# Kernel tuning notes

Hardware: AMD Instinct MI355X
Metric: run time of the kernel (lower is better)

## Reference

```python
import jax, jax.numpy as jnp
import numpy as np

C_M, C_Z, C = 256, 128, 32
N_SEQ, N_RES = 128, 256


def setup_inputs() -> dict:
    key = jax.random.key(0)
    ks = jax.random.split(key, 9)
    s = 0.02
    return {
        "m": jax.random.normal(ks[0], (N_SEQ, N_RES, C_M), dtype=jnp.float32),
        "ln_w": jnp.ones((C_M,), dtype=jnp.float32),
        "ln_b": jnp.zeros((C_M,), dtype=jnp.float32),
        "w1": jax.random.normal(ks[1], (C, C_M), dtype=jnp.float32) * s,
        "b1": jnp.zeros((C,), dtype=jnp.float32),
        "w2": jax.random.normal(ks[2], (C, C_M), dtype=jnp.float32) * s,
        "b2": jnp.zeros((C,), dtype=jnp.float32),
        "wo": jax.random.normal(ks[3], (C_Z, C * C), dtype=jnp.float32) * s,
        "bo": jnp.zeros((C_Z,), dtype=jnp.float32),
    }


def reference(m, ln_w, ln_b, w1, b1, w2, b2, wo, bo):
    n_seq = m.shape[-3]
    # LayerNorm over c_m
    mu = jnp.mean(m, axis=-1, keepdims=True)
    var = jnp.mean(jnp.square(m - mu), axis=-1, keepdims=True)
    mn = (m - mu) * jax.lax.rsqrt(var + 1e-5) * ln_w + ln_b
    # dual projections to c channels: [s, i, c]
    a = jnp.einsum('sim,cm->sic', mn, w1) + b1
    b = jnp.einsum('sjm,dm->sjd', mn, w2) + b2
    # outer product mean contracted over sequence axis: [i, j, c, d]
    o = jnp.einsum('sic,sjd->ijcd', a, b)
    o = o.reshape(o.shape[0], o.shape[1], C * C)
    # output projection and mean over sequences
    z = (jnp.einsum('ijk,zk->ijz', o, wo) + bo) / n_seq
    return z
```

## Files before the change

### kernel.cpp

```cpp
#include <hip/hip_runtime.h>
#include <hip/hip_bf16.h>
#include <stdint.h>

#define N_RES 256
#define CMDIM 256

typedef __attribute__((ext_vector_type(8))) short bf16x8;
typedef __attribute__((ext_vector_type(4))) float f32x4;
typedef __attribute__((ext_vector_type(2))) unsigned int u32x2;

__device__ __forceinline__ unsigned short f32_to_bf16(float f) {
    union { float f; unsigned int u; } v; v.f = f;
    unsigned int u = v.u;
    return (unsigned short)((u + 0x7FFFu + ((u >> 16) & 1u)) >> 16);
}

__device__ __forceinline__ int swz5(int x) {
    return ((x >> 2) & 7) | (((x >> 5) & 1) << 3) | ((x & 1) << 4);
}


__global__ __launch_bounds__(256) void k_ln_proj(
    const float* __restrict__ m, const float* __restrict__ lnw, const float* __restrict__ lnb,
    const float* __restrict__ w1, const float* __restrict__ b1,
    const float* __restrict__ w2, const float* __restrict__ b2,
    const float* __restrict__ wo,
    unsigned short* __restrict__ A2f, unsigned short* __restrict__ B2f,
    unsigned short* __restrict__ wof)
{
    __shared__ unsigned short mn[32 * 256];
    __shared__ unsigned short stg[2048];
    int b = blockIdx.x;
    int i = b >> 2, sblk = b & 3;
    int tid = threadIdx.x;
    int wv = tid >> 6, lane = tid & 63;
    int quad = lane >> 4, l15 = lane & 15;

    if (tid < 128) {
        int t = b * 128 + tid;
        int zo = t >> 10, k = t & 1023;
        int addr = ((zo >> 4) * 32 + (k >> 5)) * 512 + ((k >> 3) & 3) * 128 + (zo & 15) * 8 + (k & 7);
        wof[addr] = f32_to_bf16(wo[t]);
    }

    f32x4 lw = *(const f32x4*)(lnw + lane * 4);
    f32x4 lb = *(const f32x4*)(lnb + lane * 4);

    #pragma unroll
    for (int r = 0; r < 8; ++r) {
        int sl = wv * 8 + r;
        int s = sblk * 32 + sl;
        const float* row = m + ((size_t)s * N_RES + i) * CMDIM;
        f32x4 x = *(const f32x4*)(row + lane * 4);
        float s1 = x[0] + x[1] + x[2] + x[3];
        float s2 = x[0]*x[0] + x[1]*x[1] + x[2]*x[2] + x[3]*x[3];
        #pragma unroll
        for (int off = 32; off; off >>= 1) {
            s1 += __shfl_xor(s1, off);
            s2 += __shfl_xor(s2, off);
        }
        float mu = s1 * (1.0f / 256.0f);
        float var = s2 * (1.0f / 256.0f) - mu * mu;
        float rstd = rsqrtf(var + 1e-5f);
        float n0 = (x[0] - mu) * rstd * lw[0] + lb[0];
        float n1 = (x[1] - mu) * rstd * lw[1] + lb[1];
        float n2 = (x[2] - mu) * rstd * lw[2] + lb[2];
        float n3 = (x[3] - mu) * rstd * lw[3] + lb[3];
        unsigned int p0 = (unsigned)f32_to_bf16(n0) | ((unsigned)f32_to_bf16(n1) << 16);
        unsigned int p1 = (unsigned)f32_to_bf16(n2) | ((unsigned)f32_to_bf16(n3) << 16);
        int chunk = lane >> 1;
        int pos = (chunk & 16) | ((chunk ^ sl) & 15);
        unsigned int* dst = (unsigned int*)((char*)mn + sl * 512 + pos * 16 + (lane & 1) * 8);
        dst[0] = p0; dst[1] = p1;
    }

    const float* wrow = (wv < 2) ? (w1 + (size_t)(wv * 16 + l15) * 256)
                                 : (w2 + (size_t)((wv - 2) * 16 + l15) * 256);
    bf16x8 af[8];
    #pragma unroll
    for (int ks = 0; ks < 8; ++ks) {
        f32x4 lo = *(const f32x4*)(wrow + ks * 32 + quad * 8);
        f32x4 hi = *(const f32x4*)(wrow + ks * 32 + quad * 8 + 4);
        bf16x8 f;
        f[0] = (short)f32_to_bf16(lo[0]);
        f[1] = (short)f32_to_bf16(lo[1]);
        f[2] = (short)f32_to_bf16(lo[2]);
        f[3] = (short)f32_to_bf16(lo[3]);
        f[4] = (short)f32_to_bf16(hi[0]);
        f[5] = (short)f32_to_bf16(hi[1]);
        f[6] = (short)f32_to_bf16(hi[2]);
        f[7] = (short)f32_to_bf16(hi[3]);
        af[ks] = f;
    }

    __syncthreads();

    f32x4 acc[2];
    acc[0] = (f32x4){0.f, 0.f, 0.f, 0.f};
    acc[1] = (f32x4){0.f, 0.f, 0.f, 0.f};
    #pragma unroll
    for (int ks = 0; ks < 8; ++ks) {
        #pragma unroll
        for (int nb = 0; nb < 2; ++nb) {
            int sl = nb * 16 + l15;
            int chunk = ks * 4 + quad;
            int pos = (chunk & 16) | ((chunk ^ sl) & 15);
            bf16x8 bf = *(const bf16x8*)((char*)mn + sl * 512 + pos * 16);
            acc[nb] = __builtin_amdgcn_mfma_f32_16x16x32_bf16(af[ks], bf, acc[nb], 0, 0, 0);
        }
    }

    const float* bsrc = (wv < 2) ? b1 : b2;
    f32x4 bias = *(const f32x4*)(bsrc + (wv & 1) * 16 + quad * 4);
    unsigned short* sbase = stg + (wv >> 1) * 1024 + (wv & 1) * 512 + quad * 32;
    #pragma unroll
    for (int nb = 0; nb < 2; ++nb) {
        int sl = nb * 16 + l15;
        int soff = ((sl >> 3) & 3) * 128 + (sl & 7);
        #pragma unroll
        for (int reg = 0; reg < 4; ++reg)
            sbase[soff + reg * 8] = f32_to_bf16(acc[nb][reg] + bias[reg]);
    }
    __syncthreads();

    int part = tid >> 7, blk = (tid >> 6) & 1, l = tid & 63;
    unsigned short* gdst = (part ? B2f : A2f) + ((i * 2 + blk) * 4 + sblk) * 512 + l * 8;
    *(bf16x8*)gdst = *(const bf16x8*)(stg + tid * 8);
}

__global__ __launch_bounds__(256, 2) void k_fused(
    const unsigned short* __restrict__ A2f, const unsigned short* __restrict__ B2f,
    const unsigned short* __restrict__ wof, const float* __restrict__ bo,
    float* __restrict__ out)
{
    __shared__ char olds[65536];
    int bid = blockIdx.x;
    int sb = (bid & 7) * 256 + (bid >> 3);
    int bx = sb & 63, by = sb >> 6;
    int tid = threadIdx.x, wv = tid >> 6, lane = tid & 63;
    int quad = lane >> 4, l15 = lane & 15;
    int wm = wv & 1, wn = wv >> 1;

    const unsigned short* Abase = A2f + (size_t)((bx * 8 + wn * 4) * 4) * 512 + lane * 8;

    bf16x8 bn[4][4];
    #pragma unroll
    for (int nb = 0; nb < 4; ++nb)
        #pragma unroll
        for (int ks = 0; ks < 4; ++ks)
            bn[ks][nb] = *(const bf16x8*)(Abase + (size_t)(nb * 4 + ks) * 512);

    #pragma unroll
    for (int pass = 0; pass < 2; ++pass) {
        const unsigned short* Bbase = B2f + (size_t)((by * 16 + pass * 8 + wm * 4) * 4) * 512 + lane * 8;
        f32x4 acc[4][4];
        #pragma unroll
        for (int a = 0; a < 4; ++a)
            #pragma unroll
            for (int b = 0; b < 4; ++b) acc[a][b] = (f32x4){0.f, 0.f, 0.f, 0.f};

        bf16x8 am[4][4];
        #pragma unroll
        for (int mb = 0; mb < 4; ++mb)
            #pragma unroll
            for (int ks = 0; ks < 4; ++ks)
                am[ks][mb] = *(const bf16x8*)(Bbase + (size_t)(mb * 4 + ks) * 512);

        __builtin_amdgcn_s_setprio(1);
        #pragma unroll
        for (int ks = 0; ks < 4; ++ks)
            #pragma unroll
            for (int mb = 0; mb < 4; ++mb)
                #pragma unroll
                for (int nb = 0; nb < 4; ++nb)
                    acc[mb][nb] = __builtin_amdgcn_mfma_f32_16x16x32_bf16(am[ks][mb], bn[ks][nb], acc[mb][nb], 0, 0, 0);
        __builtin_amdgcn_s_setprio(0);

        #pragma unroll
        for (int mb = 0; mb < 4; ++mb) {
            int m_ = wm * 64 + mb * 16 + quad * 4;
            int d0 = m_ & 31;
            int jl = pass * 4 + (m_ >> 5);
            #pragma unroll
            for (int nb = 0; nb < 4; ++nb) {
                int n_ = wn * 64 + nb * 16 + l15;
                int c = n_ & 31, il = n_ >> 5;
                int pair = il * 8 + jl;
                int e0 = c * 32 + d0;
                int chunk = e0 >> 3;
                int phys = pair ^ swz5(chunk);
                f32x4 a4 = acc[mb][nb];
                unsigned int p0 = (unsigned)f32_to_bf16(a4[0]) | ((unsigned)f32_to_bf16(a4[1]) << 16);
                unsigned int p1 = (unsigned)f32_to_bf16(a4[2]) | ((unsigned)f32_to_bf16(a4[3]) << 16);
                u32x2 pv = {p0, p1};
                *(u32x2*)(olds + chunk * 512 + phys * 16 + (e0 & 7) * 2) = pv;
            }
        }
    }

    int zg = wv;
    const unsigned short* wbase = wof + (size_t)(zg * 64) * 512 + lane * 8;

    bf16x8 af2[6][4], bfr2[6][4];
    #pragma unroll
    for (int p = 0; p < 5; ++p)
        #pragma unroll
        for (int zb = 0; zb < 2; ++zb)
            #pragma unroll
            for (int h = 0; h < 2; ++h)
                af2[p][zb * 2 + h] = *(const bf16x8*)(wbase + (size_t)(zb * 32 + 2 * p + h) * 512);
    __builtin_amdgcn_sched_barrier(0);

    __syncthreads();

    #pragma unroll
    for (int p = 0; p < 5; ++p)
        #pragma unroll
        for (int pb = 0; pb < 2; ++pb)
            #pragma unroll
            for (int h = 0; h < 2; ++h) {
                int kt = 2 * p + h;
                int pair = pb * 16 + l15;
                int chunk = kt * 4 + quad;
                int phys = pair ^ swz5(chunk);
                bfr2[p][pb * 2 + h] = *(const bf16x8*)(olds + chunk * 512 + phys * 16);
            }
    __builtin_amdgcn_sched_barrier(0);

    f32x4 acc2[2][2];
    #pragma unroll
    for (int a = 0; a < 2; ++a)
        #pragma unroll
        for (int b = 0; b < 2; ++b) acc2[a][b] = (f32x4){0.f, 0.f, 0.f, 0.f};

    #pragma unroll
    for (int s = 0; s < 16; ++s) {
        int slot = s % 6;
        if (s < 11) {
            int t = s + 5, ps = t % 6;
            #pragma unroll
            for (int zb = 0; zb < 2; ++zb)
                #pragma unroll
                for (int h = 0; h < 2; ++h)
                    af2[ps][zb * 2 + h] = *(const bf16x8*)(wbase + (size_t)(zb * 32 + 2 * t + h) * 512);
            #pragma unroll
            for (int pb = 0; pb < 2; ++pb)
                #pragma unroll
                for (int h = 0; h < 2; ++h) {
                    int kt = 2 * t + h;
                    int pair = pb * 16 + l15;
                    int chunk = kt * 4 + quad;
                    int phys = pair ^ swz5(chunk);
                    bfr2[ps][pb * 2 + h] = *(const bf16x8*)(olds + chunk * 512 + phys * 16);
                }
            __builtin_amdgcn_sched_barrier(0);
        }
        __builtin_amdgcn_s_setprio(1);
        #pragma unroll
        for (int h = 0; h < 2; ++h)
            #pragma unroll
            for (int zb = 0; zb < 2; ++zb)
                #pragma unroll
                for (int pb = 0; pb < 2; ++pb)
                    acc2[zb][pb] = __builtin_amdgcn_mfma_f32_16x16x32_bf16(
                        af2[slot][zb * 2 + h], bfr2[slot][pb * 2 + h], acc2[zb][pb], 0, 0, 0);
        __builtin_amdgcn_s_setprio(0);
    }

    #pragma unroll
    for (int zb = 0; zb < 2; ++zb) {
        int zo = zg * 32 + zb * 16 + quad * 4;
        f32x4 b4 = *(const f32x4*)(bo + zo);
        #pragma unroll
        for (int pb = 0; pb < 2; ++pb) {
            int pair = pb * 16 + l15;
            int i = bx * 4 + (pair >> 3);
            int j = by * 8 + (pair & 7);
            f32x4 v;
            #pragma unroll
            for (int reg = 0; reg < 4; ++reg)
                v[reg] = (acc2[zb][pb][reg] + b4[reg]) * (1.0f / 128.0f);
            *(f32x4*)(out + ((size_t)(i * 256 + j)) * 128 + zo) = v;
        }
    }
}

extern "C" void kernel_launch(void* const* d_in, const int* in_sizes, int n_in,
                              void* d_out, int out_size, void* d_ws, size_t ws_size,
                              hipStream_t stream) {
    const float* m   = (const float*)d_in[0];
    const float* lnw = (const float*)d_in[1];
    const float* lnb = (const float*)d_in[2];
    const float* w1  = (const float*)d_in[3];
    const float* b1  = (const float*)d_in[4];
    const float* w2  = (const float*)d_in[5];
    const float* b2  = (const float*)d_in[6];
    const float* wo  = (const float*)d_in[7];
    const float* bo  = (const float*)d_in[8];
    float* out = (float*)d_out;
    char* ws = (char*)d_ws;

    unsigned short* wof = (unsigned short*)(ws + 32768);
    unsigned short* A2f = (unsigned short*)(ws + 32768 + 262144);
    unsigned short* B2f = (unsigned short*)(ws + 32768 + 262144 + 2097152);

    hipLaunchKernelGGL(k_ln_proj, dim3(1024), dim3(256), 0, stream,
                       m, lnw, lnb, w1, b1, w2, b2, wo, A2f, B2f, wof);
    hipLaunchKernelGGL(k_fused, dim3(2048), dim3(256), 0, stream,
                       A2f, B2f, wof, bo, out);
}
```

Before: 143.4 us.

## Double workgroup to 512 threads, split outer-product passes and K across waves

The fused kernel now uses 8 waves instead of 4. Each wave handles one of the two outer-product passes at once rather than looping over them. The output projection is split along K between wave pairs, and the partial sums are reduced through shared memory. The old software-pipelined, register-rotated weight prefetch is replaced by loading all 16 weight fragments into registers up front. This aims for more parallelism per block, at the cost of extra syncs, a shared-memory reduction, higher register pressure at launch_bounds(512,2), and less latency hiding.

```diff
diff --git a/kernel.cpp b/kernel.cpp
--- a/kernel.cpp
+++ b/kernel.cpp
@@ -128,7 +128,7 @@
     *(bf16x8*)gdst = *(const bf16x8*)(stg + tid * 8);
 }
 
-__global__ __launch_bounds__(256, 2) void k_fused(
+__global__ __launch_bounds__(512, 2) void k_fused(
     const unsigned short* __restrict__ A2f, const unsigned short* __restrict__ B2f,
     const unsigned short* __restrict__ wof, const float* __restrict__ bo,
     float* __restrict__ out)
@@ -139,93 +139,70 @@
     int bx = sb & 63, by = sb >> 6;
     int tid = threadIdx.x, wv = tid >> 6, lane = tid & 63;
     int quad = lane >> 4, l15 = lane & 15;
-    int wm = wv & 1, wn = wv >> 1;
+    int pass = wv >> 2, wm = (wv >> 1) & 1, wn = wv & 1;
 
     const unsigned short* Abase = A2f + (size_t)((bx * 8 + wn * 4) * 4) * 512 + lane * 8;
-
-    bf16x8 bn[4][4];
+    const unsigned short* Bbase = B2f + (size_t)((by * 16 + pass * 8 + wm * 4) * 4) * 512 + lane * 8;
+
+    bf16x8 bn[4][4], am[4][4];
     #pragma unroll
     for (int nb = 0; nb < 4; ++nb)
         #pragma unroll
         for (int ks = 0; ks < 4; ++ks)
             bn[ks][nb] = *(const bf16x8*)(Abase + (size_t)(nb * 4 + ks) * 512);
-
-    #pragma unroll
-    for (int pass = 0; pass < 2; ++pass) {
-        const unsigned short* Bbase = B2f + (size_t)((by * 16 + pass * 8 + wm * 4) * 4) * 512 + lane * 8;
-        f32x4 acc[4][4];
-        #pragma unroll
-        for (int a = 0; a < 4; ++a)
-            #pragma unroll
-            for (int b = 0; b < 4; ++b) acc[a][b] = (f32x4){0.f, 0.f, 0.f, 0.f};
-
-        bf16x8 am[4][4];
+    #pragma unroll
+    for (int mb = 0; mb < 4; ++mb)
+        #pragma unroll
+        for (int ks = 0; ks < 4; ++ks)
+            am[ks][mb] = *(const bf16x8*)(Bbase + (size_t)(mb * 4 + ks) * 512);
+
+    f32x4 acc[4][4];
+    #pragma unroll
+    for (int a = 0; a < 4; ++a)
+        #pragma unroll
+        for (int b = 0; b < 4; ++b) acc[a][b] = (f32x4){0.f, 0.f, 0.f, 0.f};
+
+    __builtin_amdgcn_s_setprio(1);
+    #pragma unroll
+    for (int ks = 0; ks < 4; ++ks)
         #pragma unroll
         for (int mb = 0; mb < 4; ++mb)
             #pragma unroll
-            for (int ks = 0; ks < 4; ++ks)
-                am[ks][mb] = *(const bf16x8*)(Bbase + (size_t)(mb * 4 + ks) * 512);
-
-        __builtin_amdgcn_s_setprio(1);
-        #pragma unroll
-        for (int ks = 0; ks < 4; ++ks)
-            #pragma unroll
-            for (int mb = 0; mb < 4; ++mb)
-                #pragma unroll
-                for (int nb = 0; nb < 4; ++nb)
-                    acc[mb][nb] = __builtin_amdgcn_mfma_f32_16x16x32_bf16(am[ks][mb], bn[ks][nb], acc[mb][nb], 0, 0, 0);
-        __builtin_amdgcn_s_setprio(0);
-
-        #pragma unroll
-        for (int mb = 0; mb < 4; ++mb) {
-            int m_ = wm * 64 + mb * 16 + quad * 4;
-            int d0 = m_ & 31;
-            int jl = pass * 4 + (m_ >> 5);
-            #pragma unroll
-            for (int nb = 0; nb < 4; ++nb) {
-                int n_ = wn * 64 + nb * 16 + l15;
-                int c = n_ & 31, il = n_ >> 5;
-                int pair = il * 8 + jl;
-                int e0 = c * 32 + d0;
-                int chunk = e0 >> 3;
-                int phys = pair ^ swz5(chunk);
-                f32x4 a4 = acc[mb][nb];
-                unsigned int p0 = (unsigned)f32_to_bf16(a4[0]) | ((unsigned)f32_to_bf16(a4[1]) << 16);
-                unsigned int p1 = (unsigned)f32_to_bf16(a4[2]) | ((unsigned)f32_to_bf16(a4[3]) << 16);
-                u32x2 pv = {p0, p1};
-                *(u32x2*)(olds + chunk * 512 + phys * 16 + (e0 & 7) * 2) = pv;
-            }
-        }
-    }
-
-    int zg = wv;
-    const unsigned short* wbase = wof + (size_t)(zg * 64) * 512 + lane * 8;
-
-    bf16x8 af2[6][4], bfr2[6][4];
-    #pragma unroll
-    for (int p = 0; p < 5; ++p)
-        #pragma unroll
-        for (int zb = 0; zb < 2; ++zb)
-            #pragma unroll
-            for (int h = 0; h < 2; ++h)
-                af2[p][zb * 2 + h] = *(const bf16x8*)(wbase + (size_t)(zb * 32 + 2 * p + h) * 512);
-    __builtin_amdgcn_sched_barrier(0);
-
-    __syncthreads();
-
-    #pragma unroll
-    for (int p = 0; p < 5; ++p)
-        #pragma unroll
-        for (int pb = 0; pb < 2; ++pb)
-            #pragma unroll
-            for (int h = 0; h < 2; ++h) {
-                int kt = 2 * p + h;
-                int pair = pb * 16 + l15;
-                int chunk = kt * 4 + quad;
-                int phys = pair ^ swz5(chunk);
-                bfr2[p][pb * 2 + h] = *(const bf16x8*)(olds + chunk * 512 + phys * 16);
-            }
-    __builtin_amdgcn_sched_barrier(0);
+            for (int nb = 0; nb < 4; ++nb)
+                acc[mb][nb] = __builtin_amdgcn_mfma_f32_16x16x32_bf16(am[ks][mb], bn[ks][nb], acc[mb][nb], 0, 0, 0);
+    __builtin_amdgcn_s_setprio(0);
+
+    #pragma unroll
+    for (int mb = 0; mb < 4; ++mb) {
+        int m_ = wm * 64 + mb * 16 + quad * 4;
+        int d0 = m_ & 31;
+        int jl = pass * 4 + (m_ >> 5);
+        #pragma unroll
+        for (int nb = 0; nb < 4; ++nb) {
+            int n_ = wn * 64 + nb * 16 + l15;
+            int c = n_ & 31, il = n_ >> 5;
+            int pair = il * 8 + jl;
+            int e0 = c * 32 + d0;
+            int chunk = e0 >> 3;
+            int phys = pair ^ swz5(chunk);
+            f32x4 a4 = acc[mb][nb];
+            unsigned int p0 = (unsigned)f32_to_bf16(a4[0]) | ((unsigned)f32_to_bf16(a4[1]) << 16);
+            unsigned int p1 = (unsigned)f32_to_bf16(a4[2]) | ((unsigned)f32_to_bf16(a4[3]) << 16);
+            u32x2 pv = {p0, p1};
+            *(u32x2*)(olds + chunk * 512 + phys * 16 + (e0 & 7) * 2) = pv;
+        }
+    }
+
+    int zg = wv >> 1, kh = wv & 1, kt0 = kh * 16;
+    const unsigned short* wbase = wof + lane * 8;
+    bf16x8 wreg[2][16];
+    #pragma unroll
+    for (int zb = 0; zb < 2; ++zb)
+        #pragma unroll
+        for (int kt = 0; kt < 16; ++kt)
+            wreg[zb][kt] = *(const bf16x8*)(wbase + (size_t)(((2 * zg + zb) * 32) + kt0 + kt) * 512);
+
+    __syncthreads();
 
     f32x4 acc2[2][2];
     #pragma unroll
@@ -234,53 +211,50 @@
         for (int b = 0; b < 2; ++b) acc2[a][b] = (f32x4){0.f, 0.f, 0.f, 0.f};
 
     #pragma unroll
-    for (int s = 0; s < 16; ++s) {
-        int slot = s % 6;
-        if (s < 11) {
-            int t = s + 5, ps = t % 6;
-            #pragma unroll
-            for (int zb = 0; zb < 2; ++zb)
-                #pragma unroll
-                for (int h = 0; h < 2; ++h)
-                    af2[ps][zb * 2 + h] = *(const bf16x8*)(wbase + (size_t)(zb * 32 + 2 * t + h) * 512);
-            #pragma unroll
-            for (int pb = 0; pb < 2; ++pb)
-                #pragma unroll
-                for (int h = 0; h < 2; ++h) {
-                    int kt = 2 * t + h;
-                    int pair = pb * 16 + l15;
-                    int chunk = kt * 4 + quad;
-                    int phys = pair ^ swz5(chunk);
-                    bfr2[ps][pb * 2 + h] = *(const bf16x8*)(olds + chunk * 512 + phys * 16);
-                }
-            __builtin_amdgcn_sched_barrier(0);
-        }
-        __builtin_amdgcn_s_setprio(1);
-        #pragma unroll
-        for (int h = 0; h < 2; ++h)
-            #pragma unroll
-            for (int zb = 0; zb < 2; ++zb)
-                #pragma unroll
-                for (int pb = 0; pb < 2; ++pb)
-                    acc2[zb][pb] = __builtin_amdgcn_mfma_f32_16x16x32_bf16(
-                        af2[slot][zb * 2 + h], bfr2[slot][pb * 2 + h], acc2[zb][pb], 0, 0, 0);
-        __builtin_amdgcn_s_setprio(0);
-    }
-
-    #pragma unroll
-    for (int zb = 0; zb < 2; ++zb) {
-        int zo = zg * 32 + zb * 16 + quad * 4;
-        f32x4 b4 = *(const f32x4*)(bo + zo);
+    for (int kt = 0; kt < 16; ++kt) {
+        bf16x8 bfr[2];
         #pragma unroll
         for (int pb = 0; pb < 2; ++pb) {
             int pair = pb * 16 + l15;
-            int i = bx * 4 + (pair >> 3);
-            int j = by * 8 + (pair & 7);
-            f32x4 v;
-            #pragma unroll
-            for (int reg = 0; reg < 4; ++reg)
-                v[reg] = (acc2[zb][pb][reg] + b4[reg]) * (1.0f / 128.0f);
-            *(f32x4*)(out + ((size_t)(i * 256 + j)) * 128 + zo) = v;
+            int chunk = (kt0 + kt) * 4 + quad;
+            int phys = pair ^ swz5(chunk);
+            bfr[pb] = *(const bf16x8*)(olds + chunk * 512 + phys * 16);
+        }
+        #pragma unroll
+        for (int zb = 0; zb < 2; ++zb)
+            #pragma unroll
+            for (int pb = 0; pb < 2; ++pb)
+                acc2[zb][pb] = __builtin_amdgcn_mfma_f32_16x16x32_bf16(
+                    wreg[zb][kt], bfr[pb], acc2[zb][pb], 0, 0, 0);
+    }
+
+    __syncthreads();
+    f32x4* red = (f32x4*)olds;
+    if (kh == 1) {
+        #pragma unroll
+        for (int zb = 0; zb < 2; ++zb)
+            #pragma unroll
+            for (int pb = 0; pb < 2; ++pb)
+                red[(((zg * 2 + zb) * 2 + pb) << 6) + quad * 16 + l15] = acc2[zb][pb];
+    }
+    __syncthreads();
+    if (kh == 0) {
+        #pragma unroll
+        for (int zb = 0; zb < 2; ++zb) {
+            int zo = zg * 32 + zb * 16 + quad * 4;
+            f32x4 b4 = *(const f32x4*)(bo + zo);
+            #pragma unroll
+            for (int pb = 0; pb < 2; ++pb) {
+                f32x4 part = red[(((zg * 2 + zb) * 2 + pb) << 6) + quad * 16 + l15];
+                int pair = pb * 16 + l15;
+                int i = bx * 4 + (pair >> 3);
+                int j = by * 8 + (pair & 7);
+                f32x4 v;
+                #pragma unroll
+                for (int reg = 0; reg < 4; ++reg)
+                    v[reg] = (acc2[zb][pb][reg] + part[reg] + b4[reg]) * (1.0f / 128.0f);
+                *(f32x4*)(out + ((size_t)(i * 256 + j)) * 128 + zo) = v;
+            }
         }
     }
 }
@@ -306,6 +280,6 @@
 
     hipLaunchKernelGGL(k_ln_proj, dim3(1024), dim3(256), 0, stream,
                        m, lnw, lnb, w1, b1, w2, b2, wo, A2f, B2f, wof);
-    hipLaunchKernelGGL(k_fused, dim3(2048), dim3(256), 0, stream,
+    hipLaunchKernelGGL(k_fused, dim3(2048), dim3(512), 0, stream,
                        A2f, B2f, wof, bo, out);
 }
```

Result: slower. 153.7 us (+7.2%).
